# Kernel tuning notes

Hardware: AMD Instinct MI355X
Metric: run time of the kernel (lower is better)

Reference implementation:

```python
import jax, jax.numpy as jnp
import numpy as np

D_MODEL = 1024
N_HEADS = 16
D_K = D_MODEL // N_HEADS
D_FF = 4096
B, S = 4, 2048


def setup_inputs() -> dict:
    key = jax.random.key(0)
    ks = jax.random.split(key, 16)
    s = 0.02
    inp = {
        "x": jax.random.normal(ks[0], (B, S, D_MODEL), dtype=jnp.float32),
        "wq": jax.random.normal(ks[1], (D_MODEL, D_MODEL), dtype=jnp.float32) * s,
        "bq": jnp.zeros((D_MODEL,), jnp.float32),
        "wk": jax.random.normal(ks[2], (D_MODEL, D_MODEL), dtype=jnp.float32) * s,
        "bk": jnp.zeros((D_MODEL,), jnp.float32),
        "wv": jax.random.normal(ks[3], (D_MODEL, D_MODEL), dtype=jnp.float32) * s,
        "bv": jnp.zeros((D_MODEL,), jnp.float32),
        "wo": jax.random.normal(ks[4], (D_MODEL, D_MODEL), dtype=jnp.float32) * s,
        "bo": jnp.zeros((D_MODEL,), jnp.float32),
        "w1": jax.random.normal(ks[5], (D_MODEL, D_FF), dtype=jnp.float32) * s,
        "b1": jnp.zeros((D_FF,), jnp.float32),
        "w2": jax.random.normal(ks[6], (D_FF, D_MODEL), dtype=jnp.float32) * s,
        "b2": jnp.zeros((D_MODEL,), jnp.float32),
        "ln1_g": jnp.ones((D_MODEL,), jnp.float32),
        "ln1_b": jnp.zeros((D_MODEL,), jnp.float32),
        "ln2_g": jnp.ones((D_MODEL,), jnp.float32),
        "ln2_b": jnp.zeros((D_MODEL,), jnp.float32),
    }
    return inp


def _layernorm(x, g, b, eps=1e-5):
    mu = jnp.mean(x, axis=-1, keepdims=True)
    var = jnp.mean(jnp.square(x - mu), axis=-1, keepdims=True)
    return (x - mu) * jax.lax.rsqrt(var + eps) * g + b


def _attention(h, wq, bq, wk, bk, wv, bv, wo, bo):
    b, s, _ = h.shape
    q = (h @ wq + bq).reshape(b, s, N_HEADS, D_K).transpose(0, 2, 1, 3)
    k = (h @ wk + bk).reshape(b, s, N_HEADS, D_K).transpose(0, 2, 1, 3)
    v = (h @ wv + bv).reshape(b, s, N_HEADS, D_K).transpose(0, 2, 1, 3)
    scores = jnp.einsum('bhqd,bhkd->bhqk', q, k) / jnp.sqrt(jnp.float32(D_K))
    causal = jnp.triu(jnp.ones((s, s), dtype=bool), k=1)  # True above diag
    scores = jnp.where(causal[None, None], -jnp.inf, scores)
    attn = jax.nn.softmax(scores, axis=-1)
    out = jnp.einsum('bhqk,bhkd->bhqd', attn, v)
    out = out.transpose(0, 2, 1, 3).reshape(b, s, D_MODEL)
    return out @ wo + bo


def reference(x, wq, bq, wk, bk, wv, bv, wo, bo, w1, b1, w2, b2,
              ln1_g, ln1_b, ln2_g, ln2_b):
    attn_out = _attention(_layernorm(x, ln1_g, ln1_b), wq, bq, wk, bk, wv, bv, wo, bo)
    x = x + attn_out
    h = _layernorm(x, ln2_g, ln2_b)
    ff = jax.nn.gelu(h @ w1 + b1, approximate=False) @ w2 + b2
    return x + ff
```

## Files before the change

### kernel.cpp

```cpp
#include <hip/hip_runtime.h>
#include <hip/hip_bf16.h>

#define DM   1024
#define DFF  4096
#define NB   4
#define SS   2048
#define NH   16
#define DK   64
#define MROWS (NB*SS)

typedef __attribute__((ext_vector_type(8)))  short bfx8;
typedef __attribute__((ext_vector_type(4)))  float fx4;
typedef __attribute__((ext_vector_type(16))) float fx16;
typedef unsigned int u32;
typedef unsigned short u16;

static __device__ __forceinline__ u16 f2bf(float f) {
  union { __hip_bfloat16 h; u16 u; } cv;
  cv.h = __float2bfloat16(f);
  return cv.u;
}
static __device__ __forceinline__ u32 pk2bf(float a, float b) {
  return (u32)f2bf(a) | ((u32)f2bf(b) << 16);
}

static __device__ __forceinline__ void async16(void* lds, const void* g) {
  typedef const __attribute__((address_space(1))) unsigned int* gp_t;
  typedef __attribute__((address_space(3))) unsigned int* lp_t;
  __builtin_amdgcn_global_load_lds((gp_t)g, (lp_t)lds, 16, 0, 0);
}

__global__ __launch_bounds__(256) void k_transpose_all(
    const float* __restrict__ wq, const float* __restrict__ wk,
    const float* __restrict__ wv, const float* __restrict__ wo,
    const float* __restrict__ w1, const float* __restrict__ w2,
    u16* __restrict__ wqkv, u16* __restrict__ wot,
    u16* __restrict__ w1t,  u16* __restrict__ w2t) {
  __shared__ float t[32][33];
  const int idx = blockIdx.x;
  const float* in; u16* out; int K, N, bx, by;
  if (idx < 4096) {
    const int m = idx >> 10, tl = idx & 1023;
    in  = (m == 0) ? wq : (m == 1) ? wk : (m == 2) ? wv : wo;
    out = (m < 3) ? (wqkv + (size_t)m * 1024 * 1024) : wot;
    K = 1024; N = 1024; bx = tl & 31; by = tl >> 5;
  } else if (idx < 8192) {
    const int tl = idx - 4096;
    in = w1; out = w1t; K = 1024; N = 4096; bx = tl & 127; by = tl >> 7;
  } else {
    const int tl = idx - 8192;
    in = w2; out = w2t; K = 4096; N = 1024; bx = tl & 31; by = tl >> 5;
  }
  const int n0 = bx * 32, k0 = by * 32;
  const int tx = threadIdx.x & 31, ty = threadIdx.x >> 5;
#pragma unroll
  for (int j = 0; j < 4; j++)
    t[ty + j * 8][tx] = in[(size_t)(k0 + ty + j * 8) * N + n0 + tx];
  __syncthreads();
#pragma unroll
  for (int j = 0; j < 4; j++)
    out[(size_t)(n0 + ty + j * 8) * K + k0 + tx] = f2bf(t[tx][ty + j * 8]);
}

__global__ __launch_bounds__(256) void k_layernorm(const float* __restrict__ x,
                                                   const float* __restrict__ g,
                                                   const float* __restrict__ b,
                                                   u16* __restrict__ out) {
  const int row  = blockIdx.x * 4 + (threadIdx.x >> 6);
  const int lane = threadIdx.x & 63;
  const float* xr = x + (size_t)row * DM;
  float4 vb[4];
  float s = 0.f, s2 = 0.f;
#pragma unroll
  for (int j = 0; j < 4; j++) {
    float4 v = *(const float4*)(xr + j * 256 + lane * 4);
    vb[j] = v;
    s  += v.x + v.y + v.z + v.w;
    s2 += v.x * v.x + v.y * v.y + v.z * v.z + v.w * v.w;
  }
#pragma unroll
  for (int off = 1; off < 64; off <<= 1) {
    s  += __shfl_xor(s,  off);
    s2 += __shfl_xor(s2, off);
  }
  const float mu   = s * (1.f / DM);
  const float var  = s2 * (1.f / DM) - mu * mu;
  const float rstd = rsqrtf(var + 1e-5f);
  u16* orow = out + (size_t)row * DM;
#pragma unroll
  for (int j = 0; j < 4; j++) {
    const int col = j * 256 + lane * 4;
    uint2 o;
    o.x = pk2bf((vb[j].x - mu) * rstd * g[col + 0] + b[col + 0],
                (vb[j].y - mu) * rstd * g[col + 1] + b[col + 1]);
    o.y = pk2bf((vb[j].z - mu) * rstd * g[col + 2] + b[col + 2],
                (vb[j].w - mu) * rstd * g[col + 3] + b[col + 3]);
    *(uint2*)(orow + col) = o;
  }
}

template <int EPI>
__global__ __launch_bounds__(512, 4) void k_gemm_bt(const u16* __restrict__ A,
                                                    const u16* __restrict__ BT,
                                                    const float* __restrict__ bias0,
                                                    const float* __restrict__ bias1,
                                                    const float* __restrict__ bias2,
                                                    const float* __restrict__ res,
                                                    void* __restrict__ outp,
                                                    int M, int N, int K) {
  constexpr int ABUF = 256 * 32 * 2;
  constexpr int BBUF = 128 * 32 * 2;
  __shared__ char Al[3 * ABUF];
  __shared__ char Bl[3 * BBUF];

  const int tid = threadIdx.x, wave = tid >> 6, lane = tid & 63;
  const int nwg = gridDim.x * gridDim.y;
  const int bid = blockIdx.y * gridDim.x + blockIdx.x;
  const int swz = (bid & 7) * (nwg >> 3) + (bid >> 3);
  const int m0 = (swz / gridDim.x) * 256, n0 = (swz % gridDim.x) * 128;
  const int wm = (wave >> 1) * 64, wn = (wave & 1) * 64;
  const int l31 = lane & 31, l5 = lane >> 5;
  const int psw = (l31 >> 1) & 3;

  fx16 acc[2][2];
#pragma unroll
  for (int i = 0; i < 2; i++)
#pragma unroll
    for (int j = 0; j < 2; j++)
#pragma unroll
      for (int e = 0; e < 16; e++) acc[i][j][e] = 0.f;

  const int arow = tid >> 2;
  const int aslot = ((tid & 3) ^ ((tid >> 3) & 3)) * 8;
  const u16* gA = A  + (size_t)(m0 + arow) * K + aslot;
  const u16* gB = BT + (size_t)(n0 + arow) * K + aslot;

  auto stageAB = [&](int buf, int kt) {
    async16(Al + buf * ABUF + wave * 1024,        gA + kt);
    async16(Al + buf * ABUF + 8192 + wave * 1024, gA + (size_t)128 * K + kt);
    async16(Bl + buf * BBUF + wave * 1024,        gB + kt);
  };

  const int nk = K >> 5;
  stageAB(0, 0);
  stageAB(1, 32);
  asm volatile("s_waitcnt vmcnt(3)" ::: "memory");
  __builtin_amdgcn_sched_barrier(0);
  __builtin_amdgcn_s_barrier();
  asm volatile("" ::: "memory");

  int cur = 0;
  for (int t = 0; t < nk; ++t) {
    const char* Ab = (const char*)Al + cur * ABUF;
    const char* Bb = (const char*)Bl + cur * BBUF;
    bfx8 av[2][2], bv[2][2];
#pragma unroll
    for (int mi = 0; mi < 2; mi++)
#pragma unroll
      for (int kk = 0; kk < 2; kk++)
        av[mi][kk] = *(const bfx8*)(Ab + (wm + mi * 32 + l31) * 64 +
                                    (((kk << 1) | l5) ^ psw) * 16);
#pragma unroll
    for (int ni = 0; ni < 2; ni++)
#pragma unroll
      for (int kk = 0; kk < 2; kk++)
        bv[ni][kk] = *(const bfx8*)(Bb + (wn + ni * 32 + l31) * 64 +
                                    (((kk << 1) | l5) ^ psw) * 16);
    int nb = cur + 2; if (nb >= 3) nb -= 3;
    if (t + 2 < nk) stageAB(nb, (t + 2) << 5);

    __builtin_amdgcn_s_setprio(1);
#pragma unroll
    for (int kk = 0; kk < 2; kk++)
#pragma unroll
      for (int mi = 0; mi < 2; mi++)
#pragma unroll
        for (int ni = 0; ni < 2; ni++)
          acc[mi][ni] = __builtin_amdgcn_mfma_f32_32x32x16_bf16(
              av[mi][kk], bv[ni][kk], acc[mi][ni], 0, 0, 0);
    __builtin_amdgcn_s_setprio(0);

    const int rem = nk - 1 - t;
    if (rem >= 2)      { asm volatile("s_waitcnt vmcnt(3)" ::: "memory"); }
    else if (rem == 1) { asm volatile("s_waitcnt vmcnt(0)" ::: "memory"); }
    __builtin_amdgcn_sched_barrier(0);
    if (rem > 0) __builtin_amdgcn_s_barrier();
    asm volatile("" ::: "memory");
    cur = (cur + 1 == 3) ? 0 : cur + 1;
  }
  __syncthreads();

  float* scr = (float*)(void*)Al + (size_t)wave * (33 * 32);

  auto emit32 = [&](u16* base, size_t ld, int mrow0, int ncol0, const float* v) {
#pragma unroll
    for (int r = 0; r < 16; r++)
      scr[((r & 3) + 8 * (r >> 2) + 4 * l5) * 33 + l31] = v[r];
    asm volatile("s_waitcnt lgkmcnt(0)" ::: "memory");
    __builtin_amdgcn_sched_barrier(0);
#pragma unroll
    for (int i = 0; i < 4; i++) {
      float4 q = *(const float4*)&scr[l31 * 33 + l5 * 16 + i * 4];
      uint2 o;
      o.x = pk2bf(q.x, q.y);
      o.y = pk2bf(q.z, q.w);
      *(uint2*)(base + (size_t)(mrow0 + l31) * ld + ncol0 + l5 * 16 + i * 4) = o;
    }
    asm volatile("s_waitcnt lgkmcnt(0)" ::: "memory");
    __builtin_amdgcn_sched_barrier(0);
  };

  if constexpr (EPI == 4) {
    const int reg = n0 >> 10;
    const float* bp = (reg == 0) ? bias0 : (reg == 1) ? bias1 : bias2;
    if (reg < 2) {
      u16* base = (u16*)outp + (size_t)reg * (8u * 1024 * 1024);
#pragma unroll
      for (int mi = 0; mi < 2; mi++)
#pragma unroll
        for (int ni = 0; ni < 2; ni++) {
          const float bs = bp[(n0 + wn + ni * 32 + l31) & 1023];
          float v[16];
#pragma unroll
          for (int r = 0; r < 16; r++) v[r] = acc[mi][ni][r] + bs;
          emit32(base, 1024, m0 + wm + mi * 32, (n0 + wn + ni * 32) & 1023, v);
        }
    } else {
#pragma unroll
      for (int mi = 0; mi < 2; mi++) {
        const int mbase = m0 + wm + mi * 32;
        const int bb2 = mbase >> 11;
#pragma unroll
        for (int ni = 0; ni < 2; ni++) {
          const int nl = (n0 + wn + ni * 32 + l31) & 1023;
          const float bs = bp[nl];
          const int hh = nl >> 6, d = nl & 63;
          u16* vph = (u16*)outp + 16u * 1024 * 1024 +
                     (((size_t)bb2 * NH + hh) * DK + d) * SS;
#pragma unroll
          for (int rg = 0; rg < 4; rg++) {
            const int s = (mbase + 8 * rg + 4 * l5) & 2047;
            uint2 o;
            o.x = pk2bf(acc[mi][ni][rg * 4 + 0] + bs, acc[mi][ni][rg * 4 + 1] + bs);
            o.y = pk2bf(acc[mi][ni][rg * 4 + 2] + bs, acc[mi][ni][rg * 4 + 3] + bs);
            *(uint2*)(vph + s) = o;
          }
        }
      }
    }
  } else if constexpr (EPI == 2) {
#pragma unroll
    for (int mi = 0; mi < 2; mi++)
#pragma unroll
      for (int ni = 0; ni < 2; ni++) {
        const float bs = bias0[n0 + wn + ni * 32 + l31];
        float v[16];
#pragma unroll
        for (int r = 0; r < 16; r++) {
          const float val = acc[mi][ni][r] + bs;
          v[r] = 0.5f * val * (1.f + erff(val * 0.70710678118f));
        }
        emit32((u16*)outp, N, m0 + wm + mi * 32, n0 + wn + ni * 32, v);
      }
  } else {
#pragma unroll
    for (int ni = 0; ni < 2; ni++) {
      const int n = n0 + wn + ni * 32 + l31;
      const float bs = bias0[n];
#pragma unroll
      for (int mi = 0; mi < 2; mi++) {
#pragma unroll
        for (int r = 0; r < 16; r++) {
          const int row = (r & 3) + 8 * (r >> 2) + 4 * l5;
          const size_t idx = (size_t)(m0 + wm + mi * 32 + row) * N + n;
          ((float*)outp)[idx] = res[idx] + acc[mi][ni][r] + bs;
        }
      }
    }
  }
}

__global__ __launch_bounds__(512, 4) void k_attn(const u16* __restrict__ q,
                                                 const u16* __restrict__ k,
                                                 const u16* __restrict__ vt,
                                                 u16* __restrict__ att) {
  __shared__ char sm[65536];
  const int bid = blockIdx.x;
  const int bq = 15 - (bid >> 6);
  const int bh = bid & 63;
  const int b = bh >> 4, h = bh & 15;

  const int tid = threadIdx.x, wave = tid >> 6, lane = tid & 63;
  const int g = wave >> 2, wv4 = wave & 3;
  const int la = lane & 15, lg = lane >> 4;
  const int q0 = bq * 128;

  bfx8 qf[2][2];
#pragma unroll
  for (int qt = 0; qt < 2; qt++) {
    const u16* qp = q + (size_t)(b * SS + q0 + wv4 * 32 + qt * 16 + la) * DM + h * DK + lg * 8;
#pragma unroll
    for (int f = 0; f < 2; f++) qf[qt][f] = *(const bfx8*)(qp + f * 32);
  }

  fx4 acc[2][4];
#pragma unroll
  for (int qt = 0; qt < 2; qt++)
#pragma unroll
    for (int dt = 0; dt < 4; dt++) acc[qt][dt] = fx4{0.f, 0.f, 0.f, 0.f};
  float mold[2] = {-10000.f, -10000.f};
  float lsum[2] = {0.f, 0.f};

  const int srow = lane >> 3;
  const int sslot = (lane & 7) ^ srow;
  const u16* kg0 = k  + (size_t)(b * SS + wv4 * 16 + srow) * DM + h * DK + sslot * 8;
  const u16* vg0 = vt + (size_t)((b * NH + h) * DK + wv4 * 16 + srow) * SS + sslot * 8;
  char* kbase = sm + g * 32768 + wv4 * 2048;
  char* vbase = sm + g * 32768 + 16384 + wv4 * 2048;

  const float c1 = 0.18033688f;
  const int niter = bq + 1;

  auto stage = [&](int buf, int i) {
    const int c0 = (2 * i + g) * 64;
#pragma unroll
    for (int j = 0; j < 2; j++)
      async16(kbase + buf * 8192 + j * 1024, kg0 + (size_t)(c0 + j * 8) * DM);
#pragma unroll
    for (int j = 0; j < 2; j++)
      async16(vbase + buf * 8192 + j * 1024, vg0 + (size_t)(j * 8) * SS + c0);
  };

  stage(0, 0);
  int cur = 0;
  const int sw = la & 7;

  for (int i = 0; i < niter; i++) {
    __syncthreads();
    if (i + 1 < niter) stage(cur ^ 1, i + 1);
    const int c0 = (2 * i + g) * 64;
    const bool msk = (i == niter - 1);
    const char* Kb = sm + g * 32768 + cur * 8192;
    const char* Vb = sm + g * 32768 + 16384 + cur * 8192;

    fx4 st[2][4];
    __builtin_amdgcn_s_setprio(1);
#pragma unroll
    for (int t = 0; t < 4; t++) {
      const char* kr = Kb + (size_t)(t * 16 + la) * 128;
      bfx8 kf0 = *(const bfx8*)(kr + ((0 + lg) ^ sw) * 16);
      bfx8 kf1 = *(const bfx8*)(kr + ((4 + lg) ^ sw) * 16);
#pragma unroll
      for (int qt = 0; qt < 2; qt++) {
        fx4 z = fx4{0.f, 0.f, 0.f, 0.f};
        z = __builtin_amdgcn_mfma_f32_16x16x32_bf16(kf0, qf[qt][0], z, 0, 0, 0);
        z = __builtin_amdgcn_mfma_f32_16x16x32_bf16(kf1, qf[qt][1], z, 0, 0, 0);
        st[qt][t] = z;
      }
    }
    __builtin_amdgcn_s_setprio(0);

    if (msk) {
#pragma unroll
      for (int qt = 0; qt < 2; qt++) {
        const int qir = q0 + wv4 * 32 + qt * 16 + la;
#pragma unroll
        for (int t = 0; t < 4; t++)
#pragma unroll
          for (int r = 0; r < 4; r++)
            if (c0 + t * 16 + lg * 4 + r > qir) st[qt][t][r] = -1e9f;
      }
    }

    float lmx[2];
#pragma unroll
    for (int qt = 0; qt < 2; qt++) {
      float mx = fmaxf(fmaxf(st[qt][0][0], st[qt][0][1]), fmaxf(st[qt][0][2], st[qt][0][3]));
#pragma unroll
      for (int t = 1; t < 4; t++)
        mx = fmaxf(mx, fmaxf(fmaxf(st[qt][t][0], st[qt][t][1]), fmaxf(st[qt][t][2], st[qt][t][3])));
      lmx[qt] = mx * c1;
    }
    const bool def = (lmx[0] <= mold[0] + 8.f) && (lmx[1] <= mold[1] + 8.f);
    if (!__all(def)) {
#pragma unroll
      for (int qt = 0; qt < 2; qt++) {
        float mx = lmx[qt];
        mx = fmaxf(mx, __shfl_xor(mx, 16));
        mx = fmaxf(mx, __shfl_xor(mx, 32));
        const float mnew  = fmaxf(mold[qt], mx);
        const float scale = exp2f(mold[qt] - mnew);
        mold[qt] = mnew;
        lsum[qt] *= scale;
#pragma unroll
        for (int dt = 0; dt < 4; dt++) {
          acc[qt][dt][0] *= scale; acc[qt][dt][1] *= scale;
          acc[qt][dt][2] *= scale; acc[qt][dt][3] *= scale;
        }
      }
    }
    u32 W[2][4][2];
#pragma unroll
    for (int qt = 0; qt < 2; qt++) {
      float ps = 0.f;
#pragma unroll
      for (int t = 0; t < 4; t++) {
        float p0 = exp2f(fmaf(st[qt][t][0], c1, -mold[qt]));
        float p1 = exp2f(fmaf(st[qt][t][1], c1, -mold[qt]));
        float p2 = exp2f(fmaf(st[qt][t][2], c1, -mold[qt]));
        float p3 = exp2f(fmaf(st[qt][t][3], c1, -mold[qt]));
        ps += (p0 + p1) + (p2 + p3);
        W[qt][t][0] = pk2bf(p0, p1);
        W[qt][t][1] = pk2bf(p2, p3);
      }
      lsum[qt] += ps;
    }

    const int sLo = la + ((lg & 1) << 5);
    const int sHi = sLo + 16;
    const bool tHi = (lg >> 1) & 1;
#pragma unroll
    for (int f = 0; f < 2; f++) {
      bfx8 pf[2];
#pragma unroll
      for (int qt = 0; qt < 2; qt++) {
        const u32 a0 = __shfl(W[qt][2 * f][0], sLo), b0 = __shfl(W[qt][2 * f + 1][0], sLo);
        const u32 a1 = __shfl(W[qt][2 * f][1], sLo), b1 = __shfl(W[qt][2 * f + 1][1], sLo);
        const u32 a2 = __shfl(W[qt][2 * f][0], sHi), b2 = __shfl(W[qt][2 * f + 1][0], sHi);
        const u32 a3 = __shfl(W[qt][2 * f][1], sHi), b3 = __shfl(W[qt][2 * f + 1][1], sHi);
        union { u32 u[4]; bfx8 v; } pu;
        pu.u[0] = tHi ? b0 : a0;
        pu.u[1] = tHi ? b1 : a1;
        pu.u[2] = tHi ? b2 : a2;
        pu.u[3] = tHi ? b3 : a3;
        pf[qt] = pu.v;
      }
      __builtin_amdgcn_s_setprio(1);
#pragma unroll
      for (int dt = 0; dt < 4; dt++) {
        const int row = dt * 16 + la;
        bfx8 vf = *(const bfx8*)(Vb + (size_t)row * 128 + (((f << 2) + lg) ^ sw) * 16);
        acc[0][dt] = __builtin_amdgcn_mfma_f32_16x16x32_bf16(vf, pf[0], acc[0][dt], 0, 0, 0);
        acc[1][dt] = __builtin_amdgcn_mfma_f32_16x16x32_bf16(vf, pf[1], acc[1][dt], 0, 0, 0);
      }
      __builtin_amdgcn_s_setprio(0);
    }
    cur ^= 1;
  }

#pragma unroll
  for (int qt = 0; qt < 2; qt++) {
    lsum[qt] += __shfl_xor(lsum[qt], 16);
    lsum[qt] += __shfl_xor(lsum[qt], 32);
  }

  __syncthreads();
  const int gi = wv4 * 64 + lane;
  float* scr = (float*)sm + (size_t)gi * 36;
  if (g == 1) {
#pragma unroll
    for (int qt = 0; qt < 2; qt++)
#pragma unroll
      for (int dt = 0; dt < 4; dt++)
#pragma unroll
        for (int j = 0; j < 4; j++) scr[qt * 16 + dt * 4 + j] = acc[qt][dt][j];
    scr[32] = mold[0]; scr[33] = mold[1];
    scr[34] = lsum[0]; scr[35] = lsum[1];
  }
  __syncthreads();
  if (g == 0) {
#pragma unroll
    for (int qt = 0; qt < 2; qt++) {
      const float mB = scr[32 + qt], lB = scr[34 + qt];
      const float mN = fmaxf(mold[qt], mB);
      const float sA = exp2f(mold[qt] - mN);
      const float sB = exp2f(mB - mN);
      const float inv = 1.f / (lsum[qt] * sA + lB * sB);
      u16* ob = att + (size_t)(b * SS + q0 + wv4 * 32 + qt * 16 + la) * DM + h * DK + lg * 4;
#pragma unroll
      for (int dt = 0; dt < 4; dt++) {
        float o0 = (acc[qt][dt][0] * sA + scr[qt * 16 + dt * 4 + 0] * sB) * inv;
        float o1 = (acc[qt][dt][1] * sA + scr[qt * 16 + dt * 4 + 1] * sB) * inv;
        float o2 = (acc[qt][dt][2] * sA + scr[qt * 16 + dt * 4 + 2] * sB) * inv;
        float o3 = (acc[qt][dt][3] * sA + scr[qt * 16 + dt * 4 + 3] * sB) * inv;
        uint2 o;
        o.x = pk2bf(o0, o1);
        o.y = pk2bf(o2, o3);
        *(uint2*)(ob + dt * 16) = o;
      }
    }
  }
}

extern "C" void kernel_launch(void* const* d_in, const int* in_sizes, int n_in,
                              void* d_out, int out_size, void* d_ws, size_t ws_size,
                              hipStream_t stream) {
  const float* x    = (const float*)d_in[0];
  const float* wq   = (const float*)d_in[1];
  const float* bq   = (const float*)d_in[2];
  const float* wk   = (const float*)d_in[3];
  const float* bk   = (const float*)d_in[4];
  const float* wv   = (const float*)d_in[5];
  const float* bv   = (const float*)d_in[6];
  const float* wo   = (const float*)d_in[7];
  const float* bo   = (const float*)d_in[8];
  const float* w1   = (const float*)d_in[9];
  const float* b1   = (const float*)d_in[10];
  const float* w2   = (const float*)d_in[11];
  const float* b2   = (const float*)d_in[12];
  const float* ln1g = (const float*)d_in[13];
  const float* ln1b = (const float*)d_in[14];
  const float* ln2g = (const float*)d_in[15];
  const float* ln2b = (const float*)d_in[16];
  float* out = (float*)d_out;

  char* w = (char*)d_ws;
  const size_t MB = 1024ull * 1024ull;
  u16*   wqkv = (u16*)(w + 0 * MB);
  u16*   wot  = (u16*)(w + 6 * MB);
  u16*   w1t  = (u16*)(w + 8 * MB);
  u16*   w2t  = (u16*)(w + 16 * MB);
  float* x2   = (float*)(w + 24 * MB);
  u16*   hb   = (u16*)(w + 56 * MB);
  u16*   qb   = (u16*)(w + 72 * MB);
  u16*   kb   = (u16*)(w + 88 * MB);
  u16*   vtb  = (u16*)(w + 104 * MB);
  u16*   atb  = (u16*)(w + 120 * MB);
  u16*   ffb  = (u16*)(w + 72 * MB);

  k_transpose_all<<<dim3(12288), 256, 0, stream>>>(wq, wk, wv, wo, w1, w2,
                                                   wqkv, wot, w1t, w2t);

  k_layernorm<<<MROWS / 4, 256, 0, stream>>>(x, ln1g, ln1b, hb);

  k_gemm_bt<4><<<dim3(24, 32), 512, 0, stream>>>(hb, wqkv, bq, bk, bv, nullptr, qb,
                                                 MROWS, 3 * DM, DM);

  k_attn<<<dim3(1024), 512, 0, stream>>>(qb, kb, vtb, atb);

  k_gemm_bt<1><<<dim3(8, 32), 512, 0, stream>>>(atb, wot, bo, nullptr, nullptr, x, x2,
                                                MROWS, DM, DM);

  k_layernorm<<<MROWS / 4, 256, 0, stream>>>(x2, ln2g, ln2b, hb);

  k_gemm_bt<2><<<dim3(32, 32), 512, 0, stream>>>(hb, w1t, b1, nullptr, nullptr, nullptr, ffb,
                                                 MROWS, DFF, DM);

  k_gemm_bt<1><<<dim3(8, 32), 512, 0, stream>>>(ffb, w2t, b2, nullptr, nullptr, x2, out,
                                                MROWS, DM, DFF);
}
```

Before: 445.5 us.

## Add 256x256-tile GEMM with phased double-buffered pipeline for QKV and FFN1

Adds a new GEMM kernel with 256x256 output tiles, 16x16x32 MFMA, a 64-wide K step, and a four-phase double-buffered LDS pipeline that interleaves async loads with MFMA quadrants. The QKV projection and the FFN up-projection with GELU now use it, and k_gemm_bt is reduced to the residual epilogue. The larger tile raises arithmetic intensity and cuts global traffic per FLOP. In exchange it needs 128KB of LDS, allows only 2 workgroups per CU, launches half as many workgroups, and uses more registers.

```diff
diff --git a/kernel.cpp b/kernel.cpp
--- a/kernel.cpp
+++ b/kernel.cpp
@@ -100,11 +100,214 @@
 }
 
 template <int EPI>
-__global__ __launch_bounds__(512, 4) void k_gemm_bt(const u16* __restrict__ A,
+__global__ __launch_bounds__(512, 2) void k_gemm256(const u16* __restrict__ A,
                                                     const u16* __restrict__ BT,
                                                     const float* __restrict__ bias0,
                                                     const float* __restrict__ bias1,
                                                     const float* __restrict__ bias2,
+                                                    void* __restrict__ outp,
+                                                    int M, int N, int K) {
+  __shared__ char Sl[131072];
+
+  const int tid = threadIdx.x, wave = tid >> 6, lane = tid & 63;
+  const int nwg = gridDim.x * gridDim.y;
+  const int bid = blockIdx.y * gridDim.x + blockIdx.x;
+  const int swz = (bid & 7) * (nwg >> 3) + (bid >> 3);
+  const int m0 = (swz / gridDim.x) * 256, n0 = (swz % gridDim.x) * 256;
+  const int wr = wave >> 2, wcn = wave & 3;
+  const int la = lane & 15, lg = lane >> 4;
+  const int psw = (la >> 1) & 3;
+
+  fx4 acc[8][4];
+#pragma unroll
+  for (int i = 0; i < 8; i++)
+#pragma unroll
+    for (int j = 0; j < 4; j++) acc[i][j] = fx4{0.f, 0.f, 0.f, 0.f};
+
+  const int rp  = wave * 16 + (lane >> 2);
+  const int sl  = (lane & 3) ^ ((lane >> 3) & 3);
+  const int gra = (rp >> 6) * 128 + (rp & 63);
+  const int grb = (rp >> 5) * 64 + (rp & 31);
+
+  auto stageA = [&](int buf, int mh, int kt) {
+    const u16* src = A + (size_t)(m0 + gra + mh * 64) * K + kt + sl * 8;
+    char* dst = Sl + buf * 32768 + mh * 16384 + wave * 1024;
+    async16(dst,        src);
+    async16(dst + 8192, src + 32);
+  };
+  auto stageB = [&](int buf, int nh, int kt) {
+    const u16* src = BT + (size_t)(n0 + grb + nh * 32) * K + kt + sl * 8;
+    char* dst = Sl + 65536 + buf * 32768 + nh * 16384 + wave * 1024;
+    async16(dst,        src);
+    async16(dst + 8192, src + 32);
+  };
+
+  const int nk = K >> 6;
+  stageA(0, 0, 0); stageB(0, 0, 0); stageA(0, 1, 0); stageB(0, 1, 0);
+  asm volatile("s_waitcnt vmcnt(4)" ::: "memory");
+  __builtin_amdgcn_sched_barrier(0);
+  __builtin_amdgcn_s_barrier();
+  asm volatile("" ::: "memory");
+
+  bfx8 avv[4][2], bv0[2][2], bv1[2][2];
+
+  auto readA = [&](int buf, int mh) {
+    const char* base = Sl + buf * 32768 + mh * 16384;
+#pragma unroll
+    for (int mtl = 0; mtl < 4; mtl++) {
+      const int r = wr * 64 + mtl * 16 + la;
+#pragma unroll
+      for (int kk = 0; kk < 2; kk++)
+        avv[mtl][kk] = *(const bfx8*)(base + kk * 8192 + r * 64 + ((lg ^ psw) * 16));
+    }
+  };
+  auto readB = [&](int buf, int nh, bfx8 (&bv)[2][2]) {
+    const char* base = Sl + 65536 + buf * 32768 + nh * 16384;
+#pragma unroll
+    for (int ntl = 0; ntl < 2; ntl++) {
+      const int r = wcn * 32 + ntl * 16 + la;
+#pragma unroll
+      for (int kk = 0; kk < 2; kk++)
+        bv[ntl][kk] = *(const bfx8*)(base + kk * 8192 + r * 64 + ((lg ^ psw) * 16));
+    }
+  };
+  auto quad = [&](int mh, int nh, bfx8 (&bv)[2][2]) {
+    __builtin_amdgcn_s_setprio(1);
+#pragma unroll
+    for (int kk = 0; kk < 2; kk++)
+#pragma unroll
+      for (int mtl = 0; mtl < 4; mtl++)
+#pragma unroll
+        for (int ntl = 0; ntl < 2; ntl++)
+          acc[mh * 4 + mtl][nh * 2 + ntl] = __builtin_amdgcn_mfma_f32_16x16x32_bf16(
+              avv[mtl][kk], bv[ntl][kk], acc[mh * 4 + mtl][nh * 2 + ntl], 0, 0, 0);
+    __builtin_amdgcn_s_setprio(0);
+  };
+
+#define PH_BAR_PRE()  do { __builtin_amdgcn_sched_barrier(0); __builtin_amdgcn_s_barrier(); \
+                           asm volatile("s_waitcnt lgkmcnt(0)" ::: "memory");                \
+                           __builtin_amdgcn_sched_barrier(0); } while (0)
+#define PH_BAR_POST() do { __builtin_amdgcn_sched_barrier(0); __builtin_amdgcn_s_barrier(); \
+                           asm volatile("" ::: "memory"); } while (0)
+
+#pragma unroll 1
+  for (int t = 0; t < nk; ++t) {
+    const int buf = t & 1, nbuf = buf ^ 1;
+    const bool pf = (t + 1 < nk);
+    const int nkt = (t + 1) << 6;
+    readA(buf, 0);
+    readB(buf, 0, bv0);
+    if (pf) stageA(nbuf, 0, nkt);
+    PH_BAR_PRE();
+    quad(0, 0, bv0);
+    PH_BAR_POST();
+    readB(buf, 1, bv1);
+    if (pf) stageB(nbuf, 0, nkt);
+    if (pf) { asm volatile("s_waitcnt vmcnt(4)" ::: "memory"); }
+    else    { asm volatile("s_waitcnt vmcnt(0)" ::: "memory"); }
+    PH_BAR_PRE();
+    quad(0, 1, bv1);
+    PH_BAR_POST();
+    readA(buf, 1);
+    if (pf) stageA(nbuf, 1, nkt);
+    PH_BAR_PRE();
+    quad(1, 0, bv0);
+    PH_BAR_POST();
+    if (pf) {
+      stageB(nbuf, 1, nkt);
+      asm volatile("s_waitcnt vmcnt(4)" ::: "memory");
+    }
+    PH_BAR_PRE();
+    quad(1, 1, bv1);
+    PH_BAR_POST();
+  }
+  __syncthreads();
+
+  const int wm = wr * 128, wn = wcn * 64;
+  float* scr = (float*)(void*)Sl + (size_t)wave * (68 * 16);
+
+  auto emit_bf16 = [&](u16* base, size_t ld, int mrow0, int ncol0,
+                       const float v[4][4] ) {
+#pragma unroll
+    for (int nt = 0; nt < 4; nt++)
+#pragma unroll
+      for (int vv = 0; vv < 4; vv++)
+        scr[(lg * 4 + vv) * 68 + nt * 16 + la] = v[nt][vv];
+    asm volatile("s_waitcnt lgkmcnt(0)" ::: "memory");
+    __builtin_amdgcn_sched_barrier(0);
+#pragma unroll
+    for (int p = 0; p < 4; p++) {
+      const int r  = p * 4 + (lane >> 4);
+      const int cg = lane & 15;
+      float4 q = *(const float4*)&scr[r * 68 + cg * 4];
+      uint2 o;
+      o.x = pk2bf(q.x, q.y);
+      o.y = pk2bf(q.z, q.w);
+      *(uint2*)(base + (size_t)(mrow0 + r) * ld + ncol0 + cg * 4) = o;
+    }
+    asm volatile("s_waitcnt lgkmcnt(0)" ::: "memory");
+    __builtin_amdgcn_sched_barrier(0);
+  };
+
+  if constexpr (EPI == 4) {
+    const int reg = n0 >> 10;
+    const float* bp = (reg == 0) ? bias0 : (reg == 1) ? bias1 : bias2;
+    if (reg < 2) {
+      u16* base = (u16*)outp + (size_t)reg * (8u * 1024 * 1024);
+#pragma unroll
+      for (int mt = 0; mt < 8; mt++) {
+        float v[4][4];
+#pragma unroll
+        for (int nt = 0; nt < 4; nt++) {
+          const float bs = bp[(n0 + wn + nt * 16 + la) & 1023];
+#pragma unroll
+          for (int vv = 0; vv < 4; vv++) v[nt][vv] = acc[mt][nt][vv] + bs;
+        }
+        emit_bf16(base, 1024, m0 + wm + mt * 16, (n0 + wn) & 1023, v);
+      }
+    } else {
+#pragma unroll
+      for (int nt = 0; nt < 4; nt++) {
+        const int nl = (n0 + wn + nt * 16 + la) & 1023;
+        const float bs = bp[nl];
+        const int hh = nl >> 6, d = nl & 63;
+#pragma unroll
+        for (int mt = 0; mt < 8; mt++) {
+          const int m = m0 + wm + mt * 16 + lg * 4;
+          const int bb2 = m >> 11, s = m & 2047;
+          u16* vp = (u16*)outp + 16u * 1024 * 1024 +
+                    (((size_t)bb2 * NH + hh) * DK + d) * SS + s;
+          uint2 o;
+          o.x = pk2bf(acc[mt][nt][0] + bs, acc[mt][nt][1] + bs);
+          o.y = pk2bf(acc[mt][nt][2] + bs, acc[mt][nt][3] + bs);
+          *(uint2*)vp = o;
+        }
+      }
+    }
+  } else {
+#pragma unroll
+    for (int mt = 0; mt < 8; mt++) {
+      float v[4][4];
+#pragma unroll
+      for (int nt = 0; nt < 4; nt++) {
+        const float bs = bias0[n0 + wn + nt * 16 + la];
+#pragma unroll
+        for (int vv = 0; vv < 4; vv++) {
+          const float val = acc[mt][nt][vv] + bs;
+          v[nt][vv] = 0.5f * val * (1.f + erff(val * 0.70710678118f));
+        }
+      }
+      emit_bf16((u16*)outp, N, m0 + wm + mt * 16, n0 + wn, v);
+    }
+  }
+#undef PH_BAR_PRE
+#undef PH_BAR_POST
+}
+
+template <int EPI>
+__global__ __launch_bounds__(512, 4) void k_gemm_bt(const u16* __restrict__ A,
+                                                    const u16* __restrict__ BT,
+                                                    const float* __restrict__ bias0,
                                                     const float* __restrict__ res,
                                                     void* __restrict__ outp,
                                                     int M, int N, int K) {
@@ -188,93 +391,18 @@
     asm volatile("" ::: "memory");
     cur = (cur + 1 == 3) ? 0 : cur + 1;
   }
-  __syncthreads();
-
-  float* scr = (float*)(void*)Al + (size_t)wave * (33 * 32);
-
-  auto emit32 = [&](u16* base, size_t ld, int mrow0, int ncol0, const float* v) {
-#pragma unroll
-    for (int r = 0; r < 16; r++)
-      scr[((r & 3) + 8 * (r >> 2) + 4 * l5) * 33 + l31] = v[r];
-    asm volatile("s_waitcnt lgkmcnt(0)" ::: "memory");
-    __builtin_amdgcn_sched_barrier(0);
-#pragma unroll
-    for (int i = 0; i < 4; i++) {
-      float4 q = *(const float4*)&scr[l31 * 33 + l5 * 16 + i * 4];
-      uint2 o;
-      o.x = pk2bf(q.x, q.y);
-      o.y = pk2bf(q.z, q.w);
-      *(uint2*)(base + (size_t)(mrow0 + l31) * ld + ncol0 + l5 * 16 + i * 4) = o;
-    }
-    asm volatile("s_waitcnt lgkmcnt(0)" ::: "memory");
-    __builtin_amdgcn_sched_barrier(0);
-  };
-
-  if constexpr (EPI == 4) {
-    const int reg = n0 >> 10;
-    const float* bp = (reg == 0) ? bias0 : (reg == 1) ? bias1 : bias2;
-    if (reg < 2) {
-      u16* base = (u16*)outp + (size_t)reg * (8u * 1024 * 1024);
-#pragma unroll
-      for (int mi = 0; mi < 2; mi++)
-#pragma unroll
-        for (int ni = 0; ni < 2; ni++) {
-          const float bs = bp[(n0 + wn + ni * 32 + l31) & 1023];
-          float v[16];
-#pragma unroll
-          for (int r = 0; r < 16; r++) v[r] = acc[mi][ni][r] + bs;
-          emit32(base, 1024, m0 + wm + mi * 32, (n0 + wn + ni * 32) & 1023, v);
-        }
-    } else {
-#pragma unroll
-      for (int mi = 0; mi < 2; mi++) {
-        const int mbase = m0 + wm + mi * 32;
-        const int bb2 = mbase >> 11;
-#pragma unroll
-        for (int ni = 0; ni < 2; ni++) {
-          const int nl = (n0 + wn + ni * 32 + l31) & 1023;
-          const float bs = bp[nl];
-          const int hh = nl >> 6, d = nl & 63;
-          u16* vph = (u16*)outp + 16u * 1024 * 1024 +
-                     (((size_t)bb2 * NH + hh) * DK + d) * SS;
-#pragma unroll
-          for (int rg = 0; rg < 4; rg++) {
-            const int s = (mbase + 8 * rg + 4 * l5) & 2047;
-            uint2 o;
-            o.x = pk2bf(acc[mi][ni][rg * 4 + 0] + bs, acc[mi][ni][rg * 4 + 1] + bs);
-            o.y = pk2bf(acc[mi][ni][rg * 4 + 2] + bs, acc[mi][ni][rg * 4 + 3] + bs);
-            *(uint2*)(vph + s) = o;
-          }
-        }
-      }
-    }
-  } else if constexpr (EPI == 2) {
-#pragma unroll
-    for (int mi = 0; mi < 2; mi++)
-#pragma unroll
-      for (int ni = 0; ni < 2; ni++) {
-        const float bs = bias0[n0 + wn + ni * 32 + l31];
-        float v[16];
-#pragma unroll
-        for (int r = 0; r < 16; r++) {
-          const float val = acc[mi][ni][r] + bs;
-          v[r] = 0.5f * val * (1.f + erff(val * 0.70710678118f));
-        }
-        emit32((u16*)outp, N, m0 + wm + mi * 32, n0 + wn + ni * 32, v);
-      }
-  } else {
-#pragma unroll
-    for (int ni = 0; ni < 2; ni++) {
-      const int n = n0 + wn + ni * 32 + l31;
-      const float bs = bias0[n];
-#pragma unroll
-      for (int mi = 0; mi < 2; mi++) {
-#pragma unroll
-        for (int r = 0; r < 16; r++) {
-          const int row = (r & 3) + 8 * (r >> 2) + 4 * l5;
-          const size_t idx = (size_t)(m0 + wm + mi * 32 + row) * N + n;
-          ((float*)outp)[idx] = res[idx] + acc[mi][ni][r] + bs;
-        }
+
+#pragma unroll
+  for (int ni = 0; ni < 2; ni++) {
+    const int n = n0 + wn + ni * 32 + l31;
+    const float bs = bias0[n];
+#pragma unroll
+    for (int mi = 0; mi < 2; mi++) {
+#pragma unroll
+      for (int r = 0; r < 16; r++) {
+        const int row = (r & 3) + 8 * (r >> 2) + 4 * l5;
+        const size_t idx = (size_t)(m0 + wm + mi * 32 + row) * N + n;
+        ((float*)outp)[idx] = res[idx] + acc[mi][ni][r] + bs;
       }
     }
   }
@@ -533,19 +661,19 @@
 
   k_layernorm<<<MROWS / 4, 256, 0, stream>>>(x, ln1g, ln1b, hb);
 
-  k_gemm_bt<4><<<dim3(24, 32), 512, 0, stream>>>(hb, wqkv, bq, bk, bv, nullptr, qb,
+  k_gemm256<4><<<dim3(12, 32), 512, 0, stream>>>(hb, wqkv, bq, bk, bv, qb,
                                                  MROWS, 3 * DM, DM);
 
   k_attn<<<dim3(1024), 512, 0, stream>>>(qb, kb, vtb, atb);
 
-  k_gemm_bt<1><<<dim3(8, 32), 512, 0, stream>>>(atb, wot, bo, nullptr, nullptr, x, x2,
+  k_gemm_bt<1><<<dim3(8, 32), 512, 0, stream>>>(atb, wot, bo, x, x2,
                                                 MROWS, DM, DM);
 
   k_layernorm<<<MROWS / 4, 256, 0, stream>>>(x2, ln2g, ln2b, hb);
 
-  k_gemm_bt<2><<<dim3(32, 32), 512, 0, stream>>>(hb, w1t, b1, nullptr, nullptr, nullptr, ffb,
+  k_gemm256<2><<<dim3(16, 32), 512, 0, stream>>>(hb, w1t, b1, nullptr, nullptr, ffb,
                                                  MROWS, DFF, DM);
 
-  k_gemm_bt<1><<<dim3(8, 32), 512, 0, stream>>>(ffb, w2t, b2, nullptr, nullptr, x2, out,
+  k_gemm_bt<1><<<dim3(8, 32), 512, 0, stream>>>(ffb, w2t, b2, x2, out,
                                                 MROWS, DM, DFF);
 }
```

New measurement: 431.1 us. 3.2% less time.
